# Performance work log

Measured on AMD Instinct MI355X. Metric: run time of the kernel, lower is better.

The kernel has to match this reference:

```python
import jax, jax.numpy as jnp
import numpy as np

NUM_ITERATIONS = 3


def setup_inputs() -> dict:
    key = jax.random.key(0)
    k1, k2 = jax.random.split(key)
    B, I, C, U, D = 64, 8, 2048, 32, 16
    x = jax.random.normal(k1, (B, I, C), dtype=jnp.float32)
    # W matches torch param (1, C, U, D, I) with leading 1 squeezed
    W = jax.random.normal(k2, (C, U, D, I), dtype=jnp.float32)
    return {"x": x, "W": W}


def _squash(s):
    # Faithful to the original: reduction over axis 1 of s (B, U, D),
    # which corresponds to dim=2 of the torch tensor (B, 1, U, D, 1)
    # i.e. the num_units axis (quirk of the original code, reproduced).
    mag_sq = jnp.sum(s * s, axis=1, keepdims=True)  # (B, 1, D)
    mag = jnp.sqrt(mag_sq)
    return mag_sq / (1.0 + mag_sq) * (s / mag)


def reference(x, W):
    # x: (B, in_units, in_channels); W: (C, U, D, I)
    B = x.shape[0]
    x_t = jnp.transpose(x, (0, 2, 1))  # (B, C, I)
    # u_hat[b,c,u,d] = sum_i W[c,u,d,i] * x_t[b,c,i]
    u_hat = jnp.einsum("bci,cudi->bcud", x_t, W)  # (B, C, U, D)
    b_ij = jnp.zeros(W.shape[:2], dtype=u_hat.dtype)  # (C, U)
    v = None
    for _ in range(NUM_ITERATIONS):
        c_ij = jax.nn.softmax(b_ij, axis=1)  # softmax over num_units
        s_j = jnp.einsum("cu,bcud->bud", c_ij, u_hat)  # (B, U, D)
        v = _squash(s_j)  # (B, U, D)
        # agreement: dot over D, mean over batch -> (C, U)
        b_ij = b_ij + jnp.einsum("bcud,bud->cu", u_hat, v) / B
    # torch returns v_j.squeeze(1): shape (B, U, D, 1)
    return v[..., None]
```

## Files before the change

kernel.cpp:

```cpp
#include <hip/hip_runtime.h>

typedef __attribute__((ext_vector_type(8))) short short8;
typedef __attribute__((ext_vector_type(4))) float f32x4;

__device__ __forceinline__ unsigned int f2bf1(float f) {
    union { float f; unsigned int u; } v; v.f = f;
    return (v.u + 0x7fffu + ((v.u >> 16) & 1u)) >> 16;
}
__device__ __forceinline__ unsigned int packbf(float a, float b) {
    return f2bf1(a) | (f2bf1(b) << 16);
}
__device__ __forceinline__ float2 bf2x(unsigned int p) {
    union { unsigned int u; float f; } lo, hi;
    lo.u = p << 16; hi.u = p & 0xffff0000u;
    return make_float2(lo.f, hi.f);
}

__global__ __launch_bounds__(256) void transpose_kernel(const float* __restrict__ x,
                                                        float* __restrict__ xt) {
    __shared__ float tile[64][65];
    const int bi0 = (blockIdx.x >> 5) << 6;
    const int c0  = (blockIdx.x & 31) << 6;
    const int tx = threadIdx.x & 63, ty = threadIdx.x >> 6;
#pragma unroll
    for (int p = 0; p < 16; ++p)
        tile[ty + p * 4][tx] = x[(size_t)(bi0 + ty + p * 4) * 2048 + c0 + tx];
    __syncthreads();
#pragma unroll
    for (int p = 0; p < 16; ++p)
        xt[(size_t)(c0 + ty + p * 4) * 512 + bi0 + tx] = tile[tx][ty + p * 4];
}

__global__ __launch_bounds__(256) void wconv_kernel(const float4* __restrict__ W4,
                                                    uint2* __restrict__ Wb2) {
    int n = blockIdx.x * 256 + threadIdx.x;
#pragma unroll
    for (int k = 0; k < 4; ++k) {
        int idx = n + k * 524288;
        float4 wv = W4[idx];
        Wb2[idx] = make_uint2(packbf(wv.x, wv.y), packbf(wv.z, wv.w));
    }
}

template <int UNIFORM>
__global__ __launch_bounds__(256) void smfma_kernel(const float* __restrict__ xt,
                                                    const unsigned short* __restrict__ Wb,
                                                    const float* __restrict__ cij,
                                                    float* __restrict__ part) {
    const int chunk = blockIdx.x >> 5;
    const int u     = blockIdx.x & 31;
    const int t = threadIdx.x, w = t >> 6, l = t & 63;
    const int m  = l & 15;
    const int kb = l >> 4;
    const int b  = w * 16 + m;

    f32x4 acc = {0.f, 0.f, 0.f, 0.f};
    const int c00 = chunk * 32;

#pragma unroll 4
    for (int q = 0; q < 8; ++q) {
        const int c = c00 + q * 4 + kb;
        uint4 av = *reinterpret_cast<const uint4*>(Wb + ((size_t)c * 32 + u) * 128 + m * 8);
        const float4* xp = reinterpret_cast<const float4*>(xt + ((size_t)c * 64 + b) * 8);
        float4 x0 = xp[0], x1 = xp[1];
        const float cw = UNIFORM ? 0.03125f : cij[c * 32 + u];
        uint4 bv;
        bv.x = packbf(x0.x * cw, x0.y * cw);
        bv.y = packbf(x0.z * cw, x0.w * cw);
        bv.z = packbf(x1.x * cw, x1.y * cw);
        bv.w = packbf(x1.z * cw, x1.w * cw);
        acc = __builtin_amdgcn_mfma_f32_16x16x32_bf16(
            __builtin_bit_cast(short8, av), __builtin_bit_cast(short8, bv), acc, 0, 0, 0);
    }

    *reinterpret_cast<f32x4*>(part + (size_t)blockIdx.x * 1024 + t * 4) = acc;
}

__global__ __launch_bounds__(256) void reduce_kernel(const float* __restrict__ part,
                                                     float* __restrict__ s) {
    const int tid = blockIdx.x * 256 + threadIdx.x;
    const int u = tid >> 8, w = (tid >> 6) & 3, lane = tid & 63;
    const float4* p = reinterpret_cast<const float4*>(part) + ((size_t)u * 256 + w * 64 + lane);
    float4 a = p[0];
#pragma unroll
    for (int k = 1; k < 64; ++k) {
        float4 q = p[(size_t)k * 8192];
        a.x += q.x; a.y += q.y; a.z += q.z; a.w += q.w;
    }
    const float* ap = &a.x;
    const int bcol = w * 16 + (lane & 15);
#pragma unroll
    for (int r = 0; r < 4; ++r) {
        const int d = (lane >> 4) * 4 + r;
        s[((size_t)u * 16 + d) * 64 + bcol] = ap[r];
    }
}

__global__ __launch_bounds__(256) void v_kernel2(const float* __restrict__ s,
                                                 float* __restrict__ v,
                                                 float* __restrict__ out) {
    int n = blockIdx.x * 256 + threadIdx.x;
    int b = n >> 4, d = n & 15;
    float sv[32];
    float msq = 0.f;
#pragma unroll
    for (int u = 0; u < 32; ++u) {
        sv[u] = s[(u * 16 + d) * 64 + b];
        msq += sv[u] * sv[u];
    }
    float scale = msq / ((1.f + msq) * sqrtf(msq));
#pragma unroll
    for (int u = 0; u < 32; ++u) {
        float val = sv[u] * scale;
        v[(b * 32 + u) * 16 + d] = val;
        out[(b * 32 + u) * 16 + d] = val;
    }
}

template <int FIRST>
__global__ __launch_bounds__(256) void delta_kernel9(const float* __restrict__ xt,
                                                     const unsigned short* __restrict__ Wb,
                                                     const float* __restrict__ v,
                                                     float* __restrict__ bij,
                                                     float* __restrict__ cij) {
    const int c = blockIdx.x;
    const int t = threadIdx.x;
    __shared__ float xs[512];
    __shared__ float sm[32];
    xs[t]       = xt[(size_t)c * 512 + t];
    xs[t + 256] = xt[(size_t)c * 512 + t + 256];
    __syncthreads();

    const int u = t >> 3, d0 = (t & 7) * 2;
    float4 a00, a01, a10, a11;
    {
        const uint4* W0 = reinterpret_cast<const uint4*>(Wb + ((size_t)c * 32 + u) * 128 + d0 * 8);
        uint4 h0 = W0[0], h1 = W0[1];
        float2 p;
        p = bf2x(h0.x); a00.x = p.x; a00.y = p.y;  p = bf2x(h0.y); a00.z = p.x; a00.w = p.y;
        p = bf2x(h0.z); a01.x = p.x; a01.y = p.y;  p = bf2x(h0.w); a01.z = p.x; a01.w = p.y;
        p = bf2x(h1.x); a10.x = p.x; a10.y = p.y;  p = bf2x(h1.y); a10.z = p.x; a10.w = p.y;
        p = bf2x(h1.z); a11.x = p.x; a11.y = p.y;  p = bf2x(h1.w); a11.z = p.x; a11.w = p.y;
    }
    float p0 = 0.f, p1 = 0.f;
#pragma unroll 4
    for (int b = 0; b < 64; b += 2) {
        {
            const float2 vv = *reinterpret_cast<const float2*>(v + (b * 32 + u) * 16 + d0);
            const float4 xa = *reinterpret_cast<const float4*>(xs + b * 8);
            const float4 xb = *reinterpret_cast<const float4*>(xs + b * 8 + 4);
            float uh0 = a00.x * xa.x + a00.y * xa.y + a00.z * xa.z + a00.w * xa.w
                      + a01.x * xb.x + a01.y * xb.y + a01.z * xb.z + a01.w * xb.w;
            float uh1 = a10.x * xa.x + a10.y * xa.y + a10.z * xa.z + a10.w * xa.w
                      + a11.x * xb.x + a11.y * xb.y + a11.z * xb.z + a11.w * xb.w;
            p0 += uh0 * vv.x + uh1 * vv.y;
        }
        {
            const float2 vv = *reinterpret_cast<const float2*>(v + ((b + 1) * 32 + u) * 16 + d0);
            const float4 xa = *reinterpret_cast<const float4*>(xs + (b + 1) * 8);
            const float4 xb = *reinterpret_cast<const float4*>(xs + (b + 1) * 8 + 4);
            float uh0 = a00.x * xa.x + a00.y * xa.y + a00.z * xa.z + a00.w * xa.w
                      + a01.x * xb.x + a01.y * xb.y + a01.z * xb.z + a01.w * xb.w;
            float uh1 = a10.x * xa.x + a10.y * xa.y + a10.z * xa.z + a10.w * xa.w
                      + a11.x * xb.x + a11.y * xb.y + a11.z * xb.z + a11.w * xb.w;
            p1 += uh0 * vv.x + uh1 * vv.y;
        }
    }
    float partial = p0 + p1;
    partial += __shfl_xor(partial, 1);
    partial += __shfl_xor(partial, 2);
    partial += __shfl_xor(partial, 4);
    if ((t & 7) == 0) {
        float r = partial * (1.0f / 64.0f);
        if (!FIRST) r += bij[c * 32 + u];
        bij[c * 32 + u] = r;
        sm[u] = r;
    }
    __syncthreads();
    if (t < 32) {
        float val = sm[t];
        float m = val;
#pragma unroll
        for (int mask = 16; mask >= 1; mask >>= 1) m = fmaxf(m, __shfl_xor(m, mask));
        float e = expf(val - m);
        float ssum = e;
#pragma unroll
        for (int mask = 16; mask >= 1; mask >>= 1) ssum += __shfl_xor(ssum, mask);
        cij[c * 32 + t] = e / ssum;
    }
}

extern "C" void kernel_launch(void* const* d_in, const int* in_sizes, int n_in,
                              void* d_out, int out_size, void* d_ws, size_t ws_size,
                              hipStream_t stream) {
    const float* x = (const float*)d_in[0];
    const float* W = (const float*)d_in[1];
    float* out = (float*)d_out;

    float* ws   = (float*)d_ws;
    float* xt   = ws;
    float* bij  = xt + 1048576;
    float* cij  = bij + 65536;
    float* s    = cij + 65536;
    float* v    = s + 32768;
    float* part = v + 32768;
    unsigned short* Wb = (unsigned short*)(part + 2097152);

    transpose_kernel<<<256, 256, 0, stream>>>(x, xt);
    wconv_kernel<<<2048, 256, 0, stream>>>((const float4*)W, (uint2*)Wb);

    smfma_kernel<1><<<2048, 256, 0, stream>>>(xt, Wb, cij, part);
    reduce_kernel<<<32, 256, 0, stream>>>(part, s);
    v_kernel2<<<4, 256, 0, stream>>>(s, v, out);
    delta_kernel9<1><<<2048, 256, 0, stream>>>(xt, Wb, v, bij, cij);

    smfma_kernel<0><<<2048, 256, 0, stream>>>(xt, Wb, cij, part);
    reduce_kernel<<<32, 256, 0, stream>>>(part, s);
    v_kernel2<<<4, 256, 0, stream>>>(s, v, out);
    delta_kernel9<0><<<2048, 256, 0, stream>>>(xt, Wb, v, bij, cij);

    smfma_kernel<0><<<2048, 256, 0, stream>>>(xt, Wb, cij, part);
    reduce_kernel<<<32, 256, 0, stream>>>(part, s);
    v_kernel2<<<4, 256, 0, stream>>>(s, v, out);
}
```

Before: 195.4 us.

## Move agreement update to MFMA, fuse W bf16 conversion into first pass

Replaces the scalar FP32 delta kernel with an MFMA-based kernel that contracts v (in bf16, transposed layout) against a bf16, interleaved copy of x, then dots the result with W. The softmax moves into a separate small kernel. The standalone W-to-bf16 conversion kernel is removed by folding the conversion and write-back into the first smfma pass. The aim is to cut the ALU cost of the agreement step and one full pass over W, in exchange for more bf16 rounding of v and x, extra launches, and scalar gathers of W in the new kernel.

Result: no change. 194.4 us (-0.5%).

```diff
diff --git a/kernel.cpp b/kernel.cpp
--- a/kernel.cpp
+++ b/kernel.cpp
@@ -10,14 +10,14 @@
 __device__ __forceinline__ unsigned int packbf(float a, float b) {
     return f2bf1(a) | (f2bf1(b) << 16);
 }
-__device__ __forceinline__ float2 bf2x(unsigned int p) {
-    union { unsigned int u; float f; } lo, hi;
-    lo.u = p << 16; hi.u = p & 0xffff0000u;
-    return make_float2(lo.f, hi.f);
+__device__ __forceinline__ float bf1(unsigned short h) {
+    union { unsigned int u; float f; } v; v.u = ((unsigned int)h) << 16;
+    return v.f;
 }
 
 __global__ __launch_bounds__(256) void transpose_kernel(const float* __restrict__ x,
-                                                        float* __restrict__ xt) {
+                                                        float* __restrict__ xt,
+                                                        unsigned short* __restrict__ x2b) {
     __shared__ float tile[64][65];
     const int bi0 = (blockIdx.x >> 5) << 6;
     const int c0  = (blockIdx.x & 31) << 6;
@@ -27,24 +27,34 @@
         tile[ty + p * 4][tx] = x[(size_t)(bi0 + ty + p * 4) * 2048 + c0 + tx];
     __syncthreads();
 #pragma unroll
-    for (int p = 0; p < 16; ++p)
-        xt[(size_t)(c0 + ty + p * 4) * 512 + bi0 + tx] = tile[tx][ty + p * 4];
-}
-
-__global__ __launch_bounds__(256) void wconv_kernel(const float4* __restrict__ W4,
-                                                    uint2* __restrict__ Wb2) {
-    int n = blockIdx.x * 256 + threadIdx.x;
-#pragma unroll
-    for (int k = 0; k < 4; ++k) {
-        int idx = n + k * 524288;
-        float4 wv = W4[idx];
-        Wb2[idx] = make_uint2(packbf(wv.x, wv.y), packbf(wv.z, wv.w));
-    }
-}
-
-template <int UNIFORM>
+    for (int p = 0; p < 16; ++p) {
+        const int c = c0 + ty + p * 4;
+        const int bi = bi0 + tx;
+        const float val = tile[tx][ty + p * 4];
+        xt[(size_t)c * 512 + bi] = val;
+        x2b[(size_t)c * 512 + (bi & 7) * 64 + (bi >> 3)] = (unsigned short)f2bf1(val);
+    }
+}
+
+__global__ __launch_bounds__(256) void softmax_kernel(const float* __restrict__ bij,
+                                                      float* __restrict__ cij) {
+    int c = blockIdx.x * 256 + threadIdx.x;
+    float vals[32];
+    float m = -1e30f;
+#pragma unroll
+    for (int u = 0; u < 32; ++u) { vals[u] = bij[c * 32 + u]; m = fmaxf(m, vals[u]); }
+    float ssum = 0.f;
+#pragma unroll
+    for (int u = 0; u < 32; ++u) { vals[u] = expf(vals[u] - m); ssum += vals[u]; }
+    float inv = 1.f / ssum;
+#pragma unroll
+    for (int u = 0; u < 32; ++u) cij[c * 32 + u] = vals[u] * inv;
+}
+
+template <int UNIFORM, int MODE>
 __global__ __launch_bounds__(256) void smfma_kernel(const float* __restrict__ xt,
-                                                    const unsigned short* __restrict__ Wb,
+                                                    const float* __restrict__ W,
+                                                    unsigned short* __restrict__ Wb,
                                                     const float* __restrict__ cij,
                                                     float* __restrict__ part) {
     const int chunk = blockIdx.x >> 5;
@@ -60,7 +70,17 @@
 #pragma unroll 4
     for (int q = 0; q < 8; ++q) {
         const int c = c00 + q * 4 + kb;
-        uint4 av = *reinterpret_cast<const uint4*>(Wb + ((size_t)c * 32 + u) * 128 + m * 8);
+        const size_t wofs = ((size_t)c * 32 + u) * 128 + m * 8;
+        uint4 av;
+        if (MODE == 1) {
+            const float4* Wp = reinterpret_cast<const float4*>(W + wofs);
+            float4 w0 = Wp[0], w1 = Wp[1];
+            av.x = packbf(w0.x, w0.y); av.y = packbf(w0.z, w0.w);
+            av.z = packbf(w1.x, w1.y); av.w = packbf(w1.z, w1.w);
+            if (w == 0) *reinterpret_cast<uint4*>(Wb + wofs) = av;
+        } else {
+            av = *reinterpret_cast<const uint4*>(Wb + wofs);
+        }
         const float4* xp = reinterpret_cast<const float4*>(xt + ((size_t)c * 64 + b) * 8);
         float4 x0 = xp[0], x1 = xp[1];
         const float cw = UNIFORM ? 0.03125f : cij[c * 32 + u];
@@ -96,9 +116,9 @@
     }
 }
 
-__global__ __launch_bounds__(256) void v_kernel2(const float* __restrict__ s,
-                                                 float* __restrict__ v,
-                                                 float* __restrict__ out) {
+__global__ __launch_bounds__(256) void v_kernel3(const float* __restrict__ s,
+                                                 float* __restrict__ out,
+                                                 unsigned short* __restrict__ vTb) {
     int n = blockIdx.x * 256 + threadIdx.x;
     int b = n >> 4, d = n & 15;
     float sv[32];
@@ -112,81 +132,54 @@
 #pragma unroll
     for (int u = 0; u < 32; ++u) {
         float val = sv[u] * scale;
-        v[(b * 32 + u) * 16 + d] = val;
         out[(b * 32 + u) * 16 + d] = val;
+        vTb[((size_t)u * 16 + d) * 64 + b] = (unsigned short)f2bf1(val);
     }
 }
 
 template <int FIRST>
-__global__ __launch_bounds__(256) void delta_kernel9(const float* __restrict__ xt,
-                                                     const unsigned short* __restrict__ Wb,
-                                                     const float* __restrict__ v,
-                                                     float* __restrict__ bij,
-                                                     float* __restrict__ cij) {
-    const int c = blockIdx.x;
-    const int t = threadIdx.x;
-    __shared__ float xs[512];
-    __shared__ float sm[32];
-    xs[t]       = xt[(size_t)c * 512 + t];
-    xs[t + 256] = xt[(size_t)c * 512 + t + 256];
-    __syncthreads();
-
-    const int u = t >> 3, d0 = (t & 7) * 2;
-    float4 a00, a01, a10, a11;
-    {
-        const uint4* W0 = reinterpret_cast<const uint4*>(Wb + ((size_t)c * 32 + u) * 128 + d0 * 8);
-        uint4 h0 = W0[0], h1 = W0[1];
-        float2 p;
-        p = bf2x(h0.x); a00.x = p.x; a00.y = p.y;  p = bf2x(h0.y); a00.z = p.x; a00.w = p.y;
-        p = bf2x(h0.z); a01.x = p.x; a01.y = p.y;  p = bf2x(h0.w); a01.z = p.x; a01.w = p.y;
-        p = bf2x(h1.x); a10.x = p.x; a10.y = p.y;  p = bf2x(h1.y); a10.z = p.x; a10.w = p.y;
-        p = bf2x(h1.z); a11.x = p.x; a11.y = p.y;  p = bf2x(h1.w); a11.z = p.x; a11.w = p.y;
-    }
-    float p0 = 0.f, p1 = 0.f;
-#pragma unroll 4
-    for (int b = 0; b < 64; b += 2) {
-        {
-            const float2 vv = *reinterpret_cast<const float2*>(v + (b * 32 + u) * 16 + d0);
-            const float4 xa = *reinterpret_cast<const float4*>(xs + b * 8);
-            const float4 xb = *reinterpret_cast<const float4*>(xs + b * 8 + 4);
-            float uh0 = a00.x * xa.x + a00.y * xa.y + a00.z * xa.z + a00.w * xa.w
-                      + a01.x * xb.x + a01.y * xb.y + a01.z * xb.z + a01.w * xb.w;
-            float uh1 = a10.x * xa.x + a10.y * xa.y + a10.z * xa.z + a10.w * xa.w
-                      + a11.x * xb.x + a11.y * xb.y + a11.z * xb.z + a11.w * xb.w;
-            p0 += uh0 * vv.x + uh1 * vv.y;
+__global__ __launch_bounds__(256) void delta_mfma(const unsigned short* __restrict__ x2b,
+                                                  const unsigned short* __restrict__ Wb,
+                                                  const unsigned short* __restrict__ vTb,
+                                                  float* __restrict__ bij) {
+    const int cg = blockIdx.x >> 5;
+    const int u  = blockIdx.x & 31;
+    const int t = threadIdx.x, w = t >> 6, l = t & 63;
+    const int m = l & 15, kb = l >> 4;
+    const int ci = m & 7;
+    const int chalf = m >> 3;
+
+    const uint4 a0 = *reinterpret_cast<const uint4*>(vTb + ((size_t)u * 16 + m) * 64 + kb * 8);
+    const uint4 a1 = *reinterpret_cast<const uint4*>(vTb + ((size_t)u * 16 + m) * 64 + 32 + kb * 8);
+
+#pragma unroll 2
+    for (int j = 0; j < 8; ++j) {
+        const int cpair = cg * 32 + w * 8 + j;
+        const int c = cpair * 2 + chalf;
+        const uint4 b0 = *reinterpret_cast<const uint4*>(x2b + (size_t)c * 512 + ci * 64 + kb * 8);
+        const uint4 b1 = *reinterpret_cast<const uint4*>(x2b + (size_t)c * 512 + ci * 64 + 32 + kb * 8);
+        f32x4 acc = {0.f, 0.f, 0.f, 0.f};
+        acc = __builtin_amdgcn_mfma_f32_16x16x32_bf16(
+            __builtin_bit_cast(short8, a0), __builtin_bit_cast(short8, b0), acc, 0, 0, 0);
+        acc = __builtin_amdgcn_mfma_f32_16x16x32_bf16(
+            __builtin_bit_cast(short8, a1), __builtin_bit_cast(short8, b1), acc, 0, 0, 0);
+        float dot = 0.f;
+#pragma unroll
+        for (int r = 0; r < 4; ++r) {
+            const int d = kb * 4 + r;
+            dot += acc[r] * bf1(Wb[((size_t)c * 32 + u) * 128 + d * 8 + ci]);
         }
-        {
-            const float2 vv = *reinterpret_cast<const float2*>(v + ((b + 1) * 32 + u) * 16 + d0);
-            const float4 xa = *reinterpret_cast<const float4*>(xs + (b + 1) * 8);
-            const float4 xb = *reinterpret_cast<const float4*>(xs + (b + 1) * 8 + 4);
-            float uh0 = a00.x * xa.x + a00.y * xa.y + a00.z * xa.z + a00.w * xa.w
-                      + a01.x * xb.x + a01.y * xb.y + a01.z * xb.z + a01.w * xb.w;
-            float uh1 = a10.x * xa.x + a10.y * xa.y + a10.z * xa.z + a10.w * xa.w
-                      + a11.x * xb.x + a11.y * xb.y + a11.z * xb.z + a11.w * xb.w;
-            p1 += uh0 * vv.x + uh1 * vv.y;
+        dot += __shfl_xor(dot, 16);
+        dot += __shfl_xor(dot, 32);
+        dot += __shfl_xor(dot, 1);
+        dot += __shfl_xor(dot, 2);
+        dot += __shfl_xor(dot, 4);
+        if (l == 0 || l == 8) {
+            const int cc = cpair * 2 + (l >> 3);
+            float r = dot * (1.0f / 64.0f);
+            if (!FIRST) r += bij[cc * 32 + u];
+            bij[cc * 32 + u] = r;
         }
-    }
-    float partial = p0 + p1;
-    partial += __shfl_xor(partial, 1);
-    partial += __shfl_xor(partial, 2);
-    partial += __shfl_xor(partial, 4);
-    if ((t & 7) == 0) {
-        float r = partial * (1.0f / 64.0f);
-        if (!FIRST) r += bij[c * 32 + u];
-        bij[c * 32 + u] = r;
-        sm[u] = r;
-    }
-    __syncthreads();
-    if (t < 32) {
-        float val = sm[t];
-        float m = val;
-#pragma unroll
-        for (int mask = 16; mask >= 1; mask >>= 1) m = fmaxf(m, __shfl_xor(m, mask));
-        float e = expf(val - m);
-        float ssum = e;
-#pragma unroll
-        for (int mask = 16; mask >= 1; mask >>= 1) ssum += __shfl_xor(ssum, mask);
-        cij[c * 32 + t] = e / ssum;
     }
 }
 
@@ -199,27 +192,29 @@
 
     float* ws   = (float*)d_ws;
     float* xt   = ws;
-    float* bij  = xt + 1048576;
+    float* part = xt + 1048576;
+    float* bij  = part + 2097152;
     float* cij  = bij + 65536;
     float* s    = cij + 65536;
-    float* v    = s + 32768;
-    float* part = v + 32768;
-    unsigned short* Wb = (unsigned short*)(part + 2097152);
-
-    transpose_kernel<<<256, 256, 0, stream>>>(x, xt);
-    wconv_kernel<<<2048, 256, 0, stream>>>((const float4*)W, (uint2*)Wb);
-
-    smfma_kernel<1><<<2048, 256, 0, stream>>>(xt, Wb, cij, part);
+    unsigned short* Wb  = (unsigned short*)(s + 32768);
+    unsigned short* x2b = Wb + 8388608;
+    unsigned short* vTb = x2b + 1048576;
+
+    transpose_kernel<<<256, 256, 0, stream>>>(x, xt, x2b);
+
+    smfma_kernel<1, 1><<<2048, 256, 0, stream>>>(xt, W, Wb, cij, part);
     reduce_kernel<<<32, 256, 0, stream>>>(part, s);
-    v_kernel2<<<4, 256, 0, stream>>>(s, v, out);
-    delta_kernel9<1><<<2048, 256, 0, stream>>>(xt, Wb, v, bij, cij);
-
-    smfma_kernel<0><<<2048, 256, 0, stream>>>(xt, Wb, cij, part);
+    v_kernel3<<<4, 256, 0, stream>>>(s, out, vTb);
+    delta_mfma<1><<<1024, 256, 0, stream>>>(x2b, Wb, vTb, bij);
+    softmax_kernel<<<8, 256, 0, stream>>>(bij, cij);
+
+    smfma_kernel<0, 2><<<2048, 256, 0, stream>>>(xt, W, Wb, cij, part);
     reduce_kernel<<<32, 256, 0, stream>>>(part, s);
-    v_kernel2<<<4, 256, 0, stream>>>(s, v, out);
-    delta_kernel9<0><<<2048, 256, 0, stream>>>(xt, Wb, v, bij, cij);
-
-    smfma_kernel<0><<<2048, 256, 0, stream>>>(xt, Wb, cij, part);
+    v_kernel3<<<4, 256, 0, stream>>>(s, out, vTb);
+    delta_mfma<0><<<1024, 256, 0, stream>>>(x2b, Wb, vTb, bij);
+    softmax_kernel<<<8, 256, 0, stream>>>(bij, cij);
+
+    smfma_kernel<0, 2><<<2048, 256, 0, stream>>>(xt, W, Wb, cij, part);
     reduce_kernel<<<32, 256, 0, stream>>>(part, s);
-    v_kernel2<<<4, 256, 0, stream>>>(s, v, out);
-}
+    v_kernel3<<<4, 256, 0, stream>>>(s, out, vTb);
+}
```
